# Kernel tuning notes

Measured on AMD Instinct MI355X. Metric: run time of the kernel, lower is better.

Reference implementation:

```python
import jax, jax.numpy as jnp
import numpy as np
from jax import lax

B, CIN, H, W = 8, 64, 128, 128
COUT, K, STRIDE, PAD = 128, 3, 1, 1
NLEV = 256  # 2**activation_bits == 2**weight_bits


def setup_inputs() -> dict:
    key = jax.random.key(0)
    kx, kw = jax.random.split(key)
    x = jax.random.uniform(kx, (B, CIN, H, W), dtype=jnp.float32)
    weight = jax.random.normal(kw, (COUT, CIN, K, K), dtype=jnp.float32)
    bias = jnp.zeros((COUT,), dtype=jnp.float32)
    return {"x": x, "weight": weight, "bias": bias}


def _lut_table(weight):
    # quantized weights in [0, 255], integer-valued
    qw = jnp.clip(jnp.round(weight * (NLEV - 1)), 0, NLEV - 1).astype(jnp.int32)
    iv = jnp.arange(NLEV, dtype=jnp.int32)
    # emulate torch .to(int16) wraparound (qw*i can exceed 32767)
    lut = (qw[..., None] * iv).astype(jnp.int16)          # [O, C, K, K, 256]
    # the original sums pcilt over its (c,p,q) dims for EVERY patch entry;
    # precollapse those dims: T[i, o] = sum_{c,p,q} lut[o,c,p,q,i]
    T = lut.astype(jnp.int32).sum(axis=(1, 2, 3))          # [O, 256]
    return T.T                                             # [256, O]


def reference(x, weight, bias):
    T = _lut_table(weight)                                 # [256, COUT]
    xq = jnp.clip(jnp.round(x * (NLEV - 1)), 0, NLEV - 1).astype(jnp.int32)
    xp = jnp.pad(xq, ((0, 0), (0, 0), (PAD, PAD), (PAD, PAD)))  # zero-pad; T[:,0]=0 matches
    xc = jnp.moveaxis(xp, 1, 0)                            # [CIN, B, Hp, Wp]

    # accumulate per-pixel channel sum of LUT rows: A[b,h,w,o] = sum_c T[x[b,c,h,w], o]
    A0 = jnp.zeros((xp.shape[0], xp.shape[2], xp.shape[3], COUT), dtype=jnp.int32)

    def body(acc, ch):
        return acc + T[ch], None

    A, _ = lax.scan(body, A0, xc)                          # [B, Hp, Wp, COUT]

    # k x k sliding-window sum over spatial dims = sum over all patch entries
    out = lax.reduce_window(A.astype(jnp.float32), 0.0, lax.add,
                            (1, K, K, 1), (1, STRIDE, STRIDE, 1), 'VALID')
    out = jnp.moveaxis(out, 3, 1) + bias[None, :, None, None]  # [B, COUT, OH, OW]
    return out
```

## Files before the change

### kernel.cpp

```cpp
#include <hip/hip_runtime.h>

#define CIN   64
#define HW    128
#define COUT  128
#define TH    8
#define TW    32
#define PXR   34
#define NITER 11
#define NTHR  512
#define HSTR  144
#define AKSTR 136
#define SLOT  (PXR * HSTR)

#define HM_OFF    0
#define AK_OFF    29376
#define SX_OFF    55488
#define SXP_OFF   56768
#define LDS_BYTES 60032

typedef int v4i __attribute__((ext_vector_type(4)));

__device__ __forceinline__ void wg_barrier() {
  asm volatile("s_waitcnt lgkmcnt(0)\n\ts_barrier" ::: "memory");
}

__device__ __forceinline__ int quad_sum(int v) {
  v += __builtin_amdgcn_mov_dpp(v, 0xB1, 0xF, 0xF, true);
  v += __builtin_amdgcn_mov_dpp(v, 0x4E, 0xF, 0xF, true);
  return v;
}

__global__ __launch_bounds__(512)
void build_tables(const float* __restrict__ weight, int* __restrict__ W_tab,
                  char* __restrict__ Kt_g) {
  __shared__ int qw_s[576];
  __shared__ int red_s[144];
  const int o = blockIdx.x;
  const int t = threadIdx.x;
  for (int j = t; j < 576; j += 512) {
    float w = weight[o * 576 + j];
    int q = (int)rintf(w * 255.f);
    qw_s[j] = q < 0 ? 0 : (q > 255 ? 255 : q);
  }
  __syncthreads();
  const int v = t >> 2, part = t & 3;
  const int i = 128 + v;
  int cnt = 0;
  const int j0 = part * 144;
  for (int j = j0; j < j0 + 144; ++j) cnt += (qw_s[j] * i) > 32767 ? 1 : 0;
  cnt = quad_sum(cnt);
  if (part == 0) Kt_g[o * 128 + v] = (char)(cnt - 128);
  if (t < 144)
    red_s[t] = qw_s[t * 4] + qw_s[t * 4 + 1] + qw_s[t * 4 + 2] + qw_s[t * 4 + 3];
  __syncthreads();
  if (t == 0) {
    int s = 0;
    for (int kk = 0; kk < 144; ++kk) s += red_s[kk];
    W_tab[o] = s;
  }
}

__global__ __launch_bounds__(NTHR, 4)
void pcilt_main(const float* __restrict__ x, const float* __restrict__ bias,
                const int* __restrict__ W_tab, const char* __restrict__ Kt_g,
                float* __restrict__ out) {
  __shared__ uint4 ldsv[LDS_BYTES / 16];
  char* ldsb = (char*)ldsv;
  unsigned char* HmB  = (unsigned char*)(ldsb + HM_OFF);
  unsigned char* KtB  = (unsigned char*)(ldsb + AK_OFF);
  unsigned short* AKB = (unsigned short*)(ldsb + AK_OFF);
  int* Sx             = (int*)(ldsb + SX_OFF);
  int* Sxp            = (int*)(ldsb + SXP_OFF);

  const int t   = (int)threadIdx.x;
  const int bid = (int)blockIdx.x;
  const int b  = bid & 7;
  const int k  = bid >> 3;
  const int h0 = (k >> 2) * TH;
  const int w0 = (k & 3) * TW;

  for (int i = t; i < 4096; i += NTHR)
    ((unsigned int*)KtB)[i] = ((const unsigned int*)Kt_g)[i];
  {
    const uint4 z4 = make_uint4(0, 0, 0, 0);
    for (int i = t; i < 2 * SLOT / 16; i += NTHR) ((uint4*)HmB)[i] = z4;
  }

  const int l    = t & 15;
  const int slot = t >> 4;
  const int w    = t >> 6;
  const int kq   = (t >> 4) & 3;
  const int we   = t & 31;
  const int og   = t >> 5;

  float wf[8], bi[8];
#pragma unroll
  for (int m = 0; m < 8; ++m) {
    wf[m] = (float)W_tab[og * 8 + m];
    bi[m] = bias[og * 8 + m];
  }

  wg_barrier();

  v4i bfr[4][2];
  const int Mt = w >> 1, Nh = w & 1;
  if (w < 6) {
#pragma unroll
    for (int nt = 0; nt < 4; ++nt)
#pragma unroll
      for (int k64 = 0; k64 < 2; ++k64)
        bfr[nt][k64] = *(const v4i*)(KtB + (Nh * 64 + nt * 16 + l) * 128 +
                                     k64 * 64 + kq * 16);
  }

  float pf0[4], pf1[4];
  int qv[2][8];
  const float* xb = x + ((size_t)b * CIN + l * 4) * (HW * HW);
  const size_t cs = (size_t)HW * HW;

#define ISSUE(rn)                                                              \
  {                                                                            \
    const int iy  = h0 + (rn)-1;                                               \
    const int iyc = iy < 0 ? 0 : (iy > 127 ? 127 : iy);                        \
    const bool rok = (iy >= 0) && (iy < HW);                                   \
    int ix = w0 + slot - 1;                                                    \
    int ixc = ix < 0 ? 0 : (ix > 127 ? 127 : ix);                              \
    bool ok = rok && (ix >= 0) && (ix < HW);                                   \
    const float* xp = xb + (size_t)iyc * HW + ixc;                             \
    float v0 = xp[0], v1 = xp[cs], v2 = xp[2 * cs], v3 = xp[3 * cs];           \
    pf0[0] = ok ? v0 : 0.f; pf0[1] = ok ? v1 : 0.f;                            \
    pf0[2] = ok ? v2 : 0.f; pf0[3] = ok ? v3 : 0.f;                            \
    if (slot >= 30) {                                                          \
      ix = w0 + slot + 1;                                    \
      ixc = ix > 127 ? 127 : ix;                                               \
      ok = rok && (ix < HW);                                                   \
      const float* xq = xb + (size_t)iyc * HW + ixc;                           \
      float u0 = xq[0], u1 = xq[cs], u2 = xq[2 * cs], u3 = xq[3 * cs];         \
      pf1[0] = ok ? u0 : 0.f; pf1[1] = ok ? u1 : 0.f;                          \
      pf1[2] = ok ? u2 : 0.f; pf1[3] = ok ? u3 : 0.f;                          \
    }                                                                          \
  }

#define QUANT4(pf, qn, base, px, sxpb)                                         \
  {                                                                            \
    int q;                                                                     \
    q = (int)rintf((pf)[0] * 255.f); (qn)[(base)+0] = q < 0 ? 0 : (q > 255 ? 255 : q); \
    q = (int)rintf((pf)[1] * 255.f); (qn)[(base)+1] = q < 0 ? 0 : (q > 255 ? 255 : q); \
    q = (int)rintf((pf)[2] * 255.f); (qn)[(base)+2] = q < 0 ? 0 : (q > 255 ? 255 : q); \
    q = (int)rintf((pf)[3] * 255.f); (qn)[(base)+3] = q < 0 ? 0 : (q > 255 ? 255 : q); \
    int pk = (((qn)[(base)+0] > 128) + ((qn)[(base)+1] > 128) +                \
              ((qn)[(base)+2] > 128) + ((qn)[(base)+3] > 128));                \
    pk = (pk << 20) + (qn)[(base)+0] + (qn)[(base)+1] + (qn)[(base)+2] + (qn)[(base)+3]; \
    pk = quad_sum(pk);                                                         \
    if ((l & 3) == 0) Sxp[(sxpb) + (px)*12 + (l >> 2)] = pk;                   \
  }

#define HIST4(q0, q1, q2, q3, px, Hc)                                          \
  {                                                                            \
    unsigned char* hp = (Hc) + (px)*HSTR;                                      \
    if ((q0) > 128) { int v = (q0) - 128; atomicAdd((unsigned int*)(hp + ((v >> 2) << 2)), 1u << ((v & 3) * 8)); } \
    if ((q1) > 128) { int v = (q1) - 128; atomicAdd((unsigned int*)(hp + ((v >> 2) << 2)), 1u << ((v & 3) * 8)); } \
    if ((q2) > 128) { int v = (q2) - 128; atomicAdd((unsigned int*)(hp + ((v >> 2) << 2)), 1u << ((v & 3) * 8)); } \
    if ((q3) > 128) { int v = (q3) - 128; atomicAdd((unsigned int*)(hp + ((v >> 2) << 2)), 1u << ((v & 3) * 8)); } \
  }

  ISSUE(0);
  QUANT4(pf0, qv[0], 0, slot, 0);
  if (slot >= 30) QUANT4(pf1, qv[0], 4, slot + 2, 0);
  ISSUE(1);
  wg_barrier();

#pragma unroll
  for (int r = 0; r < NITER; ++r) {
    if (r <= 9) {
      unsigned char* Hc = HmB + (r % 6) * SLOT;
      const int* qc = qv[r & 1];
      HIST4(qc[0], qc[1], qc[2], qc[3], slot, Hc);
      if (slot >= 30) HIST4(qc[4], qc[5], qc[6], qc[7], slot + 2, Hc);
    }
    if (r >= 3 && w < 6) {
      v4i acc[4];
#pragma unroll
      for (int nt = 0; nt < 4; ++nt) acc[nt] = (v4i){0, 0, 0, 0};
      const int prow = Mt * 16 + l;
#pragma unroll
      for (int st = 0; st < 3; ++st) {
        const unsigned char* Hs = HmB + ((r - 3 + st) % 6) * SLOT +
                                  prow * HSTR + kq * 16;
#pragma unroll
        for (int k64 = 0; k64 < 2; ++k64) {
          const v4i a = *(const v4i*)(Hs + k64 * 64);
#pragma unroll
          for (int nt = 0; nt < 4; ++nt)
            acc[nt] = __builtin_amdgcn_mfma_i32_16x16x64_i8(a, bfr[nt][k64], acc[nt], 0, 0, 0);
        }
      }
      unsigned short* AKw = AKB + (r & 1) * (48 * AKSTR);
      const int pbase = Mt * 16 + kq * 4;
#pragma unroll
      for (int nt = 0; nt < 4; ++nt) {
        const int o = Nh * 64 + nt * 16 + l;
#pragma unroll
        for (int rg = 0; rg < 4; ++rg)
          AKw[(pbase + rg) * AKSTR + o] = (unsigned short)acc[nt][rg];
      }
    }
    if (w == 6 && r <= 9) {
      const int L = t - 384;
      if (L < 34) {
        const v4i sq = *(const v4i*)&Sxp[(r & 1) * (34 * 12) + L * 12];
        Sx[(r & 7) * 40 + L] = sq.x + sq.y + sq.z + sq.w;
      }
    }
    if (w == 7 && r <= 7) {
      uint4* Hn = (uint4*)(HmB + ((r + 2) % 6) * SLOT);
      const uint4 z4 = make_uint4(0, 0, 0, 0);
      for (int i2 = t - 448; i2 < SLOT / 16; i2 += 64) Hn[i2] = z4;
    }
    if (r <= 8) {
      const int sxpb = ((r + 1) & 1) * (34 * 12);
      int* qn = qv[(r + 1) & 1];
      QUANT4(pf0, qn, 0, slot, sxpb);
      if (slot >= 30) QUANT4(pf1, qn, 4, slot + 2, sxpb);
    }
    if (r <= 7) ISSUE(r + 2);

    wg_barrier();

    if (r >= 3) {
      const int h = h0 + r - 3;
      const unsigned short* AKr = AKB + (r & 1) * (48 * AKSTR);
      int v9 = 0;
#pragma unroll
      for (int q = 0; q < 3; ++q) {
        const int sl = (r - 3 + q) & 7;
        v9 += Sx[sl * 40 + we] + Sx[sl * 40 + we + 1] + Sx[sl * 40 + we + 2];
      }
      const int sx9 = v9 & 0xFFFFF;
      const int sh9 = v9 >> 20;
      int k0 = 0, k1 = 0, k2 = 0, k3 = 0, k4 = 0, k5 = 0, k6 = 0, k7 = 0;
#pragma unroll
      for (int dx = 0; dx < 3; ++dx) {
        const uint4 p = *(const uint4*)&AKr[(we + dx) * AKSTR + og * 8];
        k0 += (int)(short)(p.x & 0xffffu); k1 += (int)(short)(p.x >> 16);
        k2 += (int)(short)(p.y & 0xffffu); k3 += (int)(short)(p.y >> 16);
        k4 += (int)(short)(p.z & 0xffffu); k5 += (int)(short)(p.z >> 16);
        k6 += (int)(short)(p.w & 0xffffu); k7 += (int)(short)(p.w >> 16);
      }
      const int kc = 128 * sh9;
      const float sxf = (float)sx9;
      float* op = out + (((size_t)b * COUT + og * 8) * HW + h) * HW + (w0 + we);
      const size_t os = (size_t)HW * HW;
      op[0 * os] = sxf * wf[0] - 65536.f * (float)(k0 + kc) + bi[0];
      op[1 * os] = sxf * wf[1] - 65536.f * (float)(k1 + kc) + bi[1];
      op[2 * os] = sxf * wf[2] - 65536.f * (float)(k2 + kc) + bi[2];
      op[3 * os] = sxf * wf[3] - 65536.f * (float)(k3 + kc) + bi[3];
      op[4 * os] = sxf * wf[4] - 65536.f * (float)(k4 + kc) + bi[4];
      op[5 * os] = sxf * wf[5] - 65536.f * (float)(k5 + kc) + bi[5];
      op[6 * os] = sxf * wf[6] - 65536.f * (float)(k6 + kc) + bi[6];
      op[7 * os] = sxf * wf[7] - 65536.f * (float)(k7 + kc) + bi[7];
    }
  }
}

extern "C" void kernel_launch(void* const* d_in, const int* in_sizes, int n_in,
                              void* d_out, int out_size, void* d_ws, size_t ws_size,
                              hipStream_t stream) {
  const float* x      = (const float*)d_in[0];
  const float* weight = (const float*)d_in[1];
  const float* bias   = (const float*)d_in[2];
  float* out = (float*)d_out;

  int*  W_tab = (int*)d_ws;
  char* Kt_g  = (char*)d_ws + 512;

  build_tables<<<128, 512, 0, stream>>>(weight, W_tab, Kt_g);

  pcilt_main<<<512, NTHR, 0, stream>>>(x, bias, W_tab, Kt_g, out);
}
```

Baseline: 44.45 us.

## Pre-sum histograms horizontally so MFMA output is final, dropping AK LDS staging

```diff
diff --git a/kernel.cpp b/kernel.cpp
--- a/kernel.cpp
+++ b/kernel.cpp
@@ -5,18 +5,18 @@
 #define COUT  128
 #define TH    8
 #define TW    32
-#define PXR   34
-#define NITER 11
+#define NITER 12
 #define NTHR  512
 #define HSTR  144
-#define AKSTR 136
-#define SLOT  (PXR * HSTR)
+#define SLOT  (34 * HSTR)
+#define H3SL  (32 * HSTR)
 
 #define HM_OFF    0
-#define AK_OFF    29376
-#define SX_OFF    55488
-#define SXP_OFF   56768
-#define LDS_BYTES 60032
+#define H3_OFF    19584
+#define SX_OFF    38016
+#define SXP_OFF   39296
+#define SX9_OFF   42560
+#define LDS_BYTES 42880
 
 typedef int v4i __attribute__((ext_vector_type(4)));
 
@@ -66,11 +66,12 @@
                 float* __restrict__ out) {
   __shared__ uint4 ldsv[LDS_BYTES / 16];
   char* ldsb = (char*)ldsv;
-  unsigned char* HmB  = (unsigned char*)(ldsb + HM_OFF);
-  unsigned char* KtB  = (unsigned char*)(ldsb + AK_OFF);
-  unsigned short* AKB = (unsigned short*)(ldsb + AK_OFF);
-  int* Sx             = (int*)(ldsb + SX_OFF);
-  int* Sxp            = (int*)(ldsb + SXP_OFF);
+  unsigned char* HmB = (unsigned char*)(ldsb + HM_OFF);
+  unsigned char* H3B = (unsigned char*)(ldsb + H3_OFF);
+  unsigned char* KtB = (unsigned char*)(ldsb + H3_OFF);
+  int* Sx  = (int*)(ldsb + SX_OFF);
+  int* Sxp = (int*)(ldsb + SXP_OFF);
+  int* Sx9 = (int*)(ldsb + SX9_OFF);
 
   const int t   = (int)threadIdx.x;
   const int bid = (int)blockIdx.x;
@@ -83,35 +84,19 @@
     ((unsigned int*)KtB)[i] = ((const unsigned int*)Kt_g)[i];
   {
     const uint4 z4 = make_uint4(0, 0, 0, 0);
-    for (int i = t; i < 2 * SLOT / 16; i += NTHR) ((uint4*)HmB)[i] = z4;
+    for (int i = t; i < SLOT / 16; i += NTHR) ((uint4*)HmB)[i] = z4;
   }
 
   const int l    = t & 15;
   const int slot = t >> 4;
-  const int w    = t >> 6;
+  const int wv   = t >> 6;
   const int kq   = (t >> 4) & 3;
-  const int we   = t & 31;
-  const int og   = t >> 5;
-
-  float wf[8], bi[8];
-#pragma unroll
-  for (int m = 0; m < 8; ++m) {
-    wf[m] = (float)W_tab[og * 8 + m];
-    bi[m] = bias[og * 8 + m];
-  }
-
-  wg_barrier();
-
-  v4i bfr[4][2];
-  const int Mt = w >> 1, Nh = w & 1;
-  if (w < 6) {
-#pragma unroll
-    for (int nt = 0; nt < 4; ++nt)
-#pragma unroll
-      for (int k64 = 0; k64 < 2; ++k64)
-        bfr[nt][k64] = *(const v4i*)(KtB + (Nh * 64 + nt * 16 + l) * 128 +
-                                     k64 * 64 + kq * 16);
-  }
+  const int Mt   = wv >> 2;
+  const int Nh   = wv & 3;
+  const int o0   = Nh * 32 + l;
+
+  const float wfo0 = (float)W_tab[o0],      bio0 = bias[o0];
+  const float wfo1 = (float)W_tab[o0 + 16], bio1 = bias[o0 + 16];
 
   float pf0[4], pf1[4];
   int qv[2][8];
@@ -165,6 +150,15 @@
   }
 
   ISSUE(0);
+  wg_barrier();
+
+  v4i bfr[2][2];
+#pragma unroll
+  for (int nt = 0; nt < 2; ++nt)
+#pragma unroll
+    for (int k64 = 0; k64 < 2; ++k64)
+      bfr[nt][k64] = *(const v4i*)(KtB + (o0 + nt * 16) * 128 + k64 * 64 + kq * 16);
+
   QUANT4(pf0, qv[0], 0, slot, 0);
   if (slot >= 30) QUANT4(pf1, qv[0], 4, slot + 2, 0);
   ISSUE(1);
@@ -173,52 +167,73 @@
 #pragma unroll
   for (int r = 0; r < NITER; ++r) {
     if (r <= 9) {
-      unsigned char* Hc = HmB + (r % 6) * SLOT;
+      unsigned char* Hc = HmB + (r & 3) * SLOT;
       const int* qc = qv[r & 1];
       HIST4(qc[0], qc[1], qc[2], qc[3], slot, Hc);
       if (slot >= 30) HIST4(qc[4], qc[5], qc[6], qc[7], slot + 2, Hc);
     }
-    if (r >= 3 && w < 6) {
-      v4i acc[4];
-#pragma unroll
-      for (int nt = 0; nt < 4; ++nt) acc[nt] = (v4i){0, 0, 0, 0};
-      const int prow = Mt * 16 + l;
+    if (r >= 1 && r <= 10 && t < 256) {
+      const int px = t & 31, ch = (t >> 5) * 16;
+      const unsigned char* hs = HmB + ((r - 1) & 3) * SLOT + px * HSTR + ch;
+      const uint4 a0 = *(const uint4*)hs;
+      const uint4 a1 = *(const uint4*)(hs + HSTR);
+      const uint4 a2 = *(const uint4*)(hs + 2 * HSTR);
+      uint4 s;
+      s.x = a0.x + a1.x + a2.x; s.y = a0.y + a1.y + a2.y;
+      s.z = a0.z + a1.z + a2.z; s.w = a0.w + a1.w + a2.w;
+      *(uint4*)(H3B + ((r - 1) & 3) * H3SL + px * HSTR + ch) = s;
+    }
+    if (r >= 4) {
+      v4i acc0 = (v4i){0, 0, 0, 0}, acc1 = (v4i){0, 0, 0, 0};
 #pragma unroll
       for (int st = 0; st < 3; ++st) {
-        const unsigned char* Hs = HmB + ((r - 3 + st) % 6) * SLOT +
-                                  prow * HSTR + kq * 16;
+        const unsigned char* Hs = H3B + ((r - 4 + st) & 3) * H3SL +
+                                  (Mt * 16 + l) * HSTR + kq * 16;
 #pragma unroll
         for (int k64 = 0; k64 < 2; ++k64) {
           const v4i a = *(const v4i*)(Hs + k64 * 64);
-#pragma unroll
-          for (int nt = 0; nt < 4; ++nt)
-            acc[nt] = __builtin_amdgcn_mfma_i32_16x16x64_i8(a, bfr[nt][k64], acc[nt], 0, 0, 0);
+          acc0 = __builtin_amdgcn_mfma_i32_16x16x64_i8(a, bfr[0][k64], acc0, 0, 0, 0);
+          acc1 = __builtin_amdgcn_mfma_i32_16x16x64_i8(a, bfr[1][k64], acc1, 0, 0, 0);
         }
       }
-      unsigned short* AKw = AKB + (r & 1) * (48 * AKSTR);
-      const int pbase = Mt * 16 + kq * 4;
-#pragma unroll
-      for (int nt = 0; nt < 4; ++nt) {
-        const int o = Nh * 64 + nt * 16 + l;
-#pragma unroll
-        for (int rg = 0; rg < 4; ++rg)
-          AKw[(pbase + rg) * AKSTR + o] = (unsigned short)acc[nt][rg];
-      }
-    }
-    if (w == 6 && r <= 9) {
-      const int L = t - 384;
+      const int j = r - 4, h = h0 + j, px0 = Mt * 16 + kq * 4;
+      const v4i s9 = *(const v4i*)&Sx9[(j & 1) * 40 + px0];
+      float4 u0, u1;
+#pragma unroll
+      for (int rg = 0; rg < 4; ++rg) {
+        const int sx = s9[rg] & 0xFFFFF;
+        const int sh = s9[rg] >> 20;
+        ((float*)&u0)[rg] = (float)sx * wfo0 - 65536.f * (float)(acc0[rg] + (sh << 7)) + bio0;
+        ((float*)&u1)[rg] = (float)sx * wfo1 - 65536.f * (float)(acc1[rg] + (sh << 7)) + bio1;
+      }
+      float* op = out + (((size_t)b * COUT + o0) * HW + h) * HW + w0 + px0;
+      *(float4*)op = u0;
+      *(float4*)(op + 16 * (size_t)(HW * HW)) = u1;
+    }
+    if (r <= 9 && wv == 7) {
+      const int L = t - 448;
       if (L < 34) {
-        const v4i sq = *(const v4i*)&Sxp[(r & 1) * (34 * 12) + L * 12];
+        const v4i sq = *(const v4i*)&Sxp[(r & 1) * 408 + L * 12];
         Sx[(r & 7) * 40 + L] = sq.x + sq.y + sq.z + sq.w;
       }
     }
-    if (w == 7 && r <= 7) {
-      uint4* Hn = (uint4*)(HmB + ((r + 2) % 6) * SLOT);
+    if (r >= 3 && r <= 10 && wv == 6 && (t & 32)) {
+      const int L = t - 416;
+      int v9 = 0;
+#pragma unroll
+      for (int q = 0; q < 3; ++q) {
+        const int sl = ((r - 3 + q) & 7) * 40;
+        v9 += Sx[sl + L] + Sx[sl + L + 1] + Sx[sl + L + 2];
+      }
+      Sx9[((r - 3) & 1) * 40 + L] = v9;
+    }
+    if (r <= 8 && wv >= 4 && wv < 6) {
+      uint4* Hn = (uint4*)(HmB + ((r + 1) & 3) * SLOT);
       const uint4 z4 = make_uint4(0, 0, 0, 0);
-      for (int i2 = t - 448; i2 < SLOT / 16; i2 += 64) Hn[i2] = z4;
+      for (int i2 = t - 256; i2 < SLOT / 16; i2 += 128) Hn[i2] = z4;
     }
     if (r <= 8) {
-      const int sxpb = ((r + 1) & 1) * (34 * 12);
+      const int sxpb = ((r + 1) & 1) * 408;
       int* qn = qv[(r + 1) & 1];
       QUANT4(pf0, qn, 0, slot, sxpb);
       if (slot >= 30) QUANT4(pf1, qn, 4, slot + 2, sxpb);
@@ -226,40 +241,6 @@
     if (r <= 7) ISSUE(r + 2);
 
     wg_barrier();
-
-    if (r >= 3) {
-      const int h = h0 + r - 3;
-      const unsigned short* AKr = AKB + (r & 1) * (48 * AKSTR);
-      int v9 = 0;
-#pragma unroll
-      for (int q = 0; q < 3; ++q) {
-        const int sl = (r - 3 + q) & 7;
-        v9 += Sx[sl * 40 + we] + Sx[sl * 40 + we + 1] + Sx[sl * 40 + we + 2];
-      }
-      const int sx9 = v9 & 0xFFFFF;
-      const int sh9 = v9 >> 20;
-      int k0 = 0, k1 = 0, k2 = 0, k3 = 0, k4 = 0, k5 = 0, k6 = 0, k7 = 0;
-#pragma unroll
-      for (int dx = 0; dx < 3; ++dx) {
-        const uint4 p = *(const uint4*)&AKr[(we + dx) * AKSTR + og * 8];
-        k0 += (int)(short)(p.x & 0xffffu); k1 += (int)(short)(p.x >> 16);
-        k2 += (int)(short)(p.y & 0xffffu); k3 += (int)(short)(p.y >> 16);
-        k4 += (int)(short)(p.z & 0xffffu); k5 += (int)(short)(p.z >> 16);
-        k6 += (int)(short)(p.w & 0xffffu); k7 += (int)(short)(p.w >> 16);
-      }
-      const int kc = 128 * sh9;
-      const float sxf = (float)sx9;
-      float* op = out + (((size_t)b * COUT + og * 8) * HW + h) * HW + (w0 + we);
-      const size_t os = (size_t)HW * HW;
-      op[0 * os] = sxf * wf[0] - 65536.f * (float)(k0 + kc) + bi[0];
-      op[1 * os] = sxf * wf[1] - 65536.f * (float)(k1 + kc) + bi[1];
-      op[2 * os] = sxf * wf[2] - 65536.f * (float)(k2 + kc) + bi[2];
-      op[3 * os] = sxf * wf[3] - 65536.f * (float)(k3 + kc) + bi[3];
-      op[4 * os] = sxf * wf[4] - 65536.f * (float)(k4 + kc) + bi[4];
-      op[5 * os] = sxf * wf[5] - 65536.f * (float)(k5 + kc) + bi[5];
-      op[6 * os] = sxf * wf[6] - 65536.f * (float)(k6 + kc) + bi[6];
-      op[7 * os] = sxf * wf[7] - 65536.f * (float)(k7 + kc) + bi[7];
-    }
   }
 }
 
```

Measured after the change: 44.34 us. No clear change (-0.3%).
